# Optimization experiments

Measured on AMD Instinct MI355X. Metric: run time of the kernel, lower is better.

Reference implementation:

```python
import jax, jax.numpy as jnp
import numpy as np

N = 100000      # num_nodes
E = 1600000     # num_edges
F_IN = 128      # node_feature_dim
D_IN = F_IN + 1 # +1 input_cards indicator
H = 128         # hidden dim (both layers)
NUM_CARDS = 110


def _xavier(key, shape):
    fan_out, fan_in = shape
    limit = np.sqrt(6.0 / (fan_in + fan_out))
    return jax.random.uniform(key, shape, jnp.float32, -limit, limit)


def setup_inputs() -> dict:
    key = jax.random.key(0)
    ks = jax.random.split(key, 12)
    x = jax.random.normal(ks[0], (N, F_IN), jnp.float32)
    edge_index = jax.random.randint(ks[1], (2, E), 0, N, jnp.int64)
    input_cards = jax.random.randint(ks[2], (N,), 0, 2, jnp.int32)
    # SAGEConv layer 1: lin_l (neighbors), lin_r (self), each [H, D_IN] + bias
    Wl1 = _xavier(ks[3], (H, D_IN)); bl1 = jnp.zeros((H,), jnp.float32)
    Wr1 = _xavier(ks[4], (H, D_IN)); br1 = jnp.zeros((H,), jnp.float32)
    # SAGEConv layer 2
    Wl2 = _xavier(ks[5], (H, H)); bl2 = jnp.zeros((H,), jnp.float32)
    Wr2 = _xavier(ks[6], (H, H)); br2 = jnp.zeros((H,), jnp.float32)
    # output layer: normal(0, 0.01)
    Wo = 0.01 * jax.random.normal(ks[7], (NUM_CARDS, H), jnp.float32)
    bo = jnp.zeros((NUM_CARDS,), jnp.float32)
    return {"x": x, "Wl1": Wl1, "bl1": bl1, "Wr1": Wr1, "br1": br1,
            "Wl2": Wl2, "bl2": bl2, "Wr2": Wr2, "br2": br2,
            "Wo": Wo, "bo": bo,
            "edge_index": edge_index, "input_cards": input_cards}


def _sage_conv_mean(h, src, dst, deg_inv, Wl, bl, Wr, br):
    # mean-aggregate source-node features at destination nodes
    summed = jax.ops.segment_sum(h[src], dst, num_segments=N)  # [N, d]
    mean = summed * deg_inv[:, None]
    return mean @ Wl.T + bl + h @ Wr.T + br


def reference(x, Wl1, bl1, Wr1, br1, Wl2, bl2, Wr2, br2, Wo, bo,
              edge_index, input_cards):
    src, dst = edge_index[0], edge_index[1]
    deg = jax.ops.segment_sum(jnp.ones((E,), jnp.float32), dst, num_segments=N)
    deg_inv = jnp.where(deg > 0, 1.0 / jnp.maximum(deg, 1.0), 0.0)
    h = jnp.concatenate([x, input_cards.astype(jnp.float32)[:, None]], axis=1)  # [N, D_IN]
    h = jax.nn.relu(_sage_conv_mean(h, src, dst, deg_inv, Wl1, bl1, Wr1, br1))
    h = jax.nn.relu(_sage_conv_mean(h, src, dst, deg_inv, Wl2, bl2, Wr2, br2))
    logits = h @ Wo.T + bo  # [N, NUM_CARDS]
    return logits
```

## Files before the change

### kernel.cpp

```cpp
#include <hip/hip_runtime.h>
#include <hip/hip_bf16.h>

#define N_NODES 100000
#define N_EDGES 1600000
#define HDIM    128
#define KCH     4
#define NUM_CARDS 110
#define NTILES  (N_NODES / 16)
#define GEMM_BLOCKS 1024

#define NB      196
#define MAXB    10240
#define PT      4096
#define PEPT    16

typedef __attribute__((ext_vector_type(8))) short bfrag;
typedef __attribute__((ext_vector_type(4))) float ffrag;
typedef __attribute__((ext_vector_type(2))) float f32x2;

__device__ inline unsigned short f2bf(float f) {
    __hip_bfloat16 h = __float2bfloat16(f);
    unsigned short u; __builtin_memcpy(&u, &h, 2); return u;
}
__device__ inline float bf_lo(unsigned int u) {
    unsigned int v = u << 16; float f; __builtin_memcpy(&f, &v, 4); return f;
}
__device__ inline float bf_hi(unsigned int u) {
    unsigned int v = u & 0xffff0000u; float f; __builtin_memcpy(&f, &v, 4); return f;
}

__device__ inline void gload_lds16(const void* g, void* l) {
    __builtin_amdgcn_global_load_lds(
        (const __attribute__((address_space(1))) unsigned int*)g,
        (__attribute__((address_space(3))) unsigned int*)l, 16, 0, 0);
}


__global__ __launch_bounds__(256) void k_partition(
    const int* __restrict__ src, const int* __restrict__ dst,
    int* __restrict__ bucket_cursor, unsigned int* __restrict__ part) {
    __shared__ int hist[NB];
    __shared__ int hcur[NB];
    const int t = threadIdx.x;
    const int base = blockIdx.x * PT;
    for (int i = t; i < NB; i += 256) hist[i] = 0;
    __syncthreads();
#pragma unroll
    for (int i = 0; i < PEPT; i++) {
        int e = base + i * 256 + t;
        if (e < N_EDGES) atomicAdd(&hist[dst[e] >> 9], 1);
    }
    __syncthreads();
    for (int b = t; b < NB; b += 256) {
        int h = hist[b];
        hcur[b] = h ? atomicAdd(&bucket_cursor[b], h) : 0;
    }
    __syncthreads();
#pragma unroll
    for (int i = 0; i < PEPT; i++) {
        int e = base + i * 256 + t;
        if (e < N_EDGES) {
            int d = dst[e];
            int b = d >> 9;
            int r = atomicAdd(&hcur[b], 1);
            if (r < MAXB)
                part[(size_t)b * MAXB + r] =
                    ((unsigned int)(d & 511) << 17) | (unsigned int)src[e];
        }
    }
}

__global__ __launch_bounds__(256) void k_bucket(
    const unsigned int* __restrict__ part, const int* __restrict__ bucket_cursor,
    int* __restrict__ row_off, int* __restrict__ deg, float* __restrict__ deg_inv,
    int* __restrict__ csr_src) {
    __shared__ int degl[512];
    __shared__ int offl[512];
    __shared__ int curl[512];
    __shared__ int stmp[256];
    const int t = threadIdx.x;
    const int b = blockIdx.x;
    const int n0 = b << 9;
    const int nb = min(512, N_NODES - n0);
    const int cnt = min(bucket_cursor[b], MAXB);
    const int row0 = b * MAXB;
    const unsigned int* pb = &part[(size_t)b * MAXB];

    degl[t] = 0; degl[t + 256] = 0;
    __syncthreads();
    for (int i = t; i < cnt; i += 256)
        atomicAdd(&degl[pb[i] >> 17], 1);
    __syncthreads();
    const int a0 = degl[2 * t], a1 = degl[2 * t + 1];
    stmp[t] = a0 + a1;
    __syncthreads();
    for (int off = 1; off < 256; off <<= 1) {
        int x = (t >= off) ? stmp[t - off] : 0;
        __syncthreads();
        stmp[t] += x;
        __syncthreads();
    }
    const int excl = stmp[t] - (a0 + a1);
    offl[2 * t] = excl;          curl[2 * t] = excl;
    offl[2 * t + 1] = excl + a0; curl[2 * t + 1] = excl + a0;
    __syncthreads();
    for (int i = t; i < nb; i += 256) {
        int n = n0 + i;
        int d = degl[i];
        row_off[n] = row0 + offl[i];
        deg[n] = d;
        deg_inv[n] = (d > 0) ? 1.0f / (float)d : 0.0f;
    }
    for (int i = t; i < cnt; i += 256) {
        unsigned int pk = pb[i];
        int r = atomicAdd(&curl[pk >> 17], 1);
        csr_src[row0 + r] = (int)(pk & 0x1FFFFu);
    }
}


__global__ void k_prep_w(const float* __restrict__ Wl1, const float* __restrict__ Wr1,
                         const float* __restrict__ bl1, const float* __restrict__ br1,
                         const float* __restrict__ Wl2, const float* __restrict__ Wr2,
                         const float* __restrict__ bl2, const float* __restrict__ br2,
                         const float* __restrict__ Wo,  const float* __restrict__ bo,
                         unsigned short* __restrict__ W1, unsigned short* __restrict__ W2,
                         unsigned short* __restrict__ Wob,
                         float* __restrict__ bias1, float* __restrict__ bias2,
                         float* __restrict__ biaso, float* __restrict__ wcard1) {
    const int j = blockIdx.x;
    const int k = threadIdx.x;
    const float* s1 = (j < 128) ? &Wl1[(size_t)j * 129] : &Wr1[(size_t)(j - 128) * 129];
    W1[(size_t)j * HDIM + k] = f2bf(s1[k]);
    const float* s2 = (j < 128) ? &Wl2[(size_t)j * HDIM] : &Wr2[(size_t)(j - 128) * HDIM];
    W2[(size_t)j * HDIM + k] = f2bf(s2[k]);
    if (j < 112)
        Wob[(size_t)j * HDIM + k] = (j < NUM_CARDS) ? f2bf(Wo[(size_t)j * HDIM + k])
                                                    : (unsigned short)0;
    if (k == 0) {
        wcard1[j] = s1[HDIM];
        bias1[j] = (j < 128) ? 0.f : (bl1[j - 128] + br1[j - 128]);
        bias2[j] = (j < 128) ? 0.f : (bl2[j - 128] + br2[j - 128]);
        if (j < 112) biaso[j] = (j < NUM_CARDS) ? bo[j] : 0.f;
    }
}


__global__ __launch_bounds__(256) void k_gemm_dual(
    const unsigned short* __restrict__ Ab, const float* __restrict__ Af,
    const int* __restrict__ cards,
    const unsigned short* __restrict__ W,
    const float* __restrict__ bias, const float* __restrict__ wcard,
    unsigned char* __restrict__ Gq, unsigned short* __restrict__ Rb,
    int layer1) {
    __shared__ __align__(16) unsigned char smem[16384 + 2048];
    float* bias_l = (float*)(smem + 16384);
    float* wc_l   = (float*)(smem + 16384 + 1024);

    const int tix  = threadIdx.x;
    const int wave = tix >> 6;
    const int lane = tix & 63;
    const int m16  = lane & 15;
    const int quad = lane >> 4;
    const int u0   = wave * 4;
    const bool isG = (wave < 2);
    const int xk   = m16 & 7;

    bfrag wf[4][KCH];
#pragma unroll
    for (int u = 0; u < 4; u++) {
        const int j = (u0 + u) * 16 + m16;
#pragma unroll
        for (int c = 0; c < KCH; c++)
            wf[u][c] = *(const bfrag*)&W[(size_t)j * HDIM + c * 32 + quad * 8];
    }

    bias_l[tix] = bias[tix];
    wc_l[tix]   = layer1 ? wcard[tix] : 0.f;

    const int sw1 = (tix ^ ((tix >> 5) & 7)) << 4;
    const int sw2 = (tix ^ ((tix >> 4) & 7)) << 4;
    const int ldsoff = wave << 10;

    int tile = blockIdx.x;
    if (layer1) {
        const unsigned char* g = (const unsigned char*)Af + (size_t)tile * 8192;
        gload_lds16(g + sw1,        smem + ldsoff);
        gload_lds16(g + sw1 + 4096, smem + 4096 + ldsoff);
    } else {
        const unsigned char* g = (const unsigned char*)Ab + (size_t)tile * 4096;
        gload_lds16(g + sw2, smem + ldsoff);
    }
    float cvn = layer1 ? (float)cards[tile * 16 + m16] : 0.f;
    __syncthreads();

    for (int buf = 0; tile < NTILES; tile += GEMM_BLOCKS, buf ^= 1) {
        const int tn = tile + GEMM_BLOCKS;
        const bool more = (tn < NTILES);
        const float cv = cvn;

        if (more) {
            if (layer1) {
                const unsigned char* g = (const unsigned char*)Af + (size_t)tn * 8192;
                unsigned char* d = smem + (buf ^ 1) * 8192 + ldsoff;
                gload_lds16(g + sw1,        d);
                gload_lds16(g + sw1 + 4096, d + 4096);
                cvn = (float)cards[tn * 16 + m16];
            } else {
                const unsigned char* g = (const unsigned char*)Ab + (size_t)tn * 4096;
                gload_lds16(g + sw2, smem + (buf ^ 1) * 4096 + ldsoff);
            }
        }

        const unsigned char* B = smem + buf * (layer1 ? 8192 : 4096);
        bfrag hf[KCH];
        if (layer1) {
#pragma unroll
            for (int c = 0; c < KCH; c++) {
                const int s0 = m16 * 32 + c * 8 + quad * 2;
                const float4 p0 = *(const float4*)(B + (((s0    ) ^ xk) << 4));
                const float4 p1 = *(const float4*)(B + (((s0 + 1) ^ xk) << 4));
                bfrag h;
                h[0] = (short)f2bf(p0.x); h[1] = (short)f2bf(p0.y);
                h[2] = (short)f2bf(p0.z); h[3] = (short)f2bf(p0.w);
                h[4] = (short)f2bf(p1.x); h[5] = (short)f2bf(p1.y);
                h[6] = (short)f2bf(p1.z); h[7] = (short)f2bf(p1.w);
                hf[c] = h;
            }
        } else {
#pragma unroll
            for (int c = 0; c < KCH; c++) {
                const int s = m16 * 16 + c * 4 + quad;
                hf[c] = *(const bfrag*)(B + ((s ^ xk) << 4));
            }
        }

        const int node = tile * 16 + m16;
#pragma unroll
        for (int u = 0; u < 4; u++) {
            ffrag acc = {0.f, 0.f, 0.f, 0.f};
#pragma unroll
            for (int c = 0; c < KCH; c++)
                acc = __builtin_amdgcn_mfma_f32_16x16x32_bf16(wf[u][c], hf[c], acc, 0, 0, 0);
            const int jj0 = (u0 + u) * 16 + quad * 4;
            const float4 b0 = *(const float4*)&bias_l[jj0];
            const float4 w0 = *(const float4*)&wc_l[jj0];
            float v[4];
            v[0] = acc[0] + b0.x + cv * w0.x;
            v[1] = acc[1] + b0.y + cv * w0.y;
            v[2] = acc[2] + b0.z + cv * w0.z;
            v[3] = acc[3] + b0.w + cv * w0.w;
            if (isG) {
                int pk = __builtin_amdgcn_cvt_pk_fp8_f32(v[0], v[1], 0, false);
                pk = __builtin_amdgcn_cvt_pk_fp8_f32(v[2], v[3], pk, true);
                *(unsigned int*)&Gq[(size_t)node * HDIM + (u0 + u) * 16 + quad * 4] =
                    (unsigned int)pk;
            } else {
                unsigned short o[4];
#pragma unroll
                for (int r = 0; r < 4; r++) o[r] = f2bf(v[r]);
                uint2 p = {(unsigned int)o[0] | ((unsigned int)o[1] << 16),
                           (unsigned int)o[2] | ((unsigned int)o[3] << 16)};
                *(uint2*)&Rb[(size_t)node * HDIM + (u0 + u - 8) * 16 + quad * 4] = p;
            }
        }

        if (more) __syncthreads();
    }
}


__global__ __launch_bounds__(256) void k_agg(
    const unsigned char* __restrict__ Gq, const unsigned short* __restrict__ Rb,
    const int* __restrict__ row_off, const int* __restrict__ deg,
    const float* __restrict__ deg_inv, const int* __restrict__ csr_src,
    unsigned short* __restrict__ outH) {
    const int wave = threadIdx.x >> 6;
    const int lane = threadIdx.x & 63;
    const int g = lane >> 3;
    const int l = lane & 7;
    const int n = (blockIdx.x * 4 + wave) * 8 + g;
    const int start = row_off[n];
    const int d = deg[n];
    const float di = deg_inv[n];
    const int fo = l * 16;

    int dmax = d;
    dmax = max(dmax, __shfl_xor(dmax, 8, 64));
    dmax = max(dmax, __shfl_xor(dmax, 16, 64));
    dmax = max(dmax, __shfl_xor(dmax, 32, 64));

    const uint4 rv0 = *(const uint4*)&Rb[(size_t)n * HDIM + fo];
    const uint4 rv1 = *(const uint4*)&Rb[(size_t)n * HDIM + fo + 8];

    f32x2 acc2[8];
#pragma unroll
    for (int i = 0; i < 8; i++) acc2[i] = (f32x2){0.f, 0.f};

    int idxA = (l < d) ? csr_src[start + l] * HDIM : 0;
    int idxB = (8 + l < d) ? csr_src[start + 8 + l] * HDIM : 0;

    uint4 cur = {0u, 0u, 0u, 0u};
    {
        const int off0 = __shfl(idxA, g << 3, 64);
        if (0 < d) cur = *(const uint4*)&Gq[(size_t)(unsigned)off0 + fo];
    }
#define ACC16(Cv)                                                        \
    acc2[0] += __builtin_amdgcn_cvt_pk_f32_fp8((int)(Cv).x, false);      \
    acc2[1] += __builtin_amdgcn_cvt_pk_f32_fp8((int)(Cv).x, true);       \
    acc2[2] += __builtin_amdgcn_cvt_pk_f32_fp8((int)(Cv).y, false);      \
    acc2[3] += __builtin_amdgcn_cvt_pk_f32_fp8((int)(Cv).y, true);       \
    acc2[4] += __builtin_amdgcn_cvt_pk_f32_fp8((int)(Cv).z, false);      \
    acc2[5] += __builtin_amdgcn_cvt_pk_f32_fp8((int)(Cv).z, true);       \
    acc2[6] += __builtin_amdgcn_cvt_pk_f32_fp8((int)(Cv).w, false);      \
    acc2[7] += __builtin_amdgcn_cvt_pk_f32_fp8((int)(Cv).w, true);

    for (int i = 1; i < dmax; i++) {
        const int sl = i & 7;
        if (sl == 0) {
            idxA = idxB;
            const int j = i + 8 + l;
            idxB = (j < d) ? csr_src[start + j] * HDIM : 0;
        }
        const int offn = __shfl(idxA, (g << 3) | sl, 64);
        uint4 nxt = {0u, 0u, 0u, 0u};
        if (i < d) nxt = *(const uint4*)&Gq[(size_t)(unsigned)offn + fo];
        ACC16(cur);
        cur = nxt;
    }
    ACC16(cur);
#undef ACC16

    const float r[16] = {bf_lo(rv0.x), bf_hi(rv0.x), bf_lo(rv0.y), bf_hi(rv0.y),
                         bf_lo(rv0.z), bf_hi(rv0.z), bf_lo(rv0.w), bf_hi(rv0.w),
                         bf_lo(rv1.x), bf_hi(rv1.x), bf_lo(rv1.y), bf_hi(rv1.y),
                         bf_lo(rv1.z), bf_hi(rv1.z), bf_lo(rv1.w), bf_hi(rv1.w)};
    unsigned short o[16];
#pragma unroll
    for (int i = 0; i < 8; i++) {
        o[2 * i]     = f2bf(fmaxf(acc2[i].x * di + r[2 * i], 0.f));
        o[2 * i + 1] = f2bf(fmaxf(acc2[i].y * di + r[2 * i + 1], 0.f));
    }
    uint4 p0, p1;
    p0.x = (unsigned int)o[0] | ((unsigned int)o[1] << 16);
    p0.y = (unsigned int)o[2] | ((unsigned int)o[3] << 16);
    p0.z = (unsigned int)o[4] | ((unsigned int)o[5] << 16);
    p0.w = (unsigned int)o[6] | ((unsigned int)o[7] << 16);
    p1.x = (unsigned int)o[8] | ((unsigned int)o[9] << 16);
    p1.y = (unsigned int)o[10] | ((unsigned int)o[11] << 16);
    p1.z = (unsigned int)o[12] | ((unsigned int)o[13] << 16);
    p1.w = (unsigned int)o[14] | ((unsigned int)o[15] << 16);
    *(uint4*)&outH[(size_t)n * HDIM + fo] = p0;
    *(uint4*)&outH[(size_t)n * HDIM + fo + 8] = p1;
}


__global__ __launch_bounds__(256) void k_gemm_logits(
    const unsigned short* __restrict__ A, const unsigned short* __restrict__ W,
    const float* __restrict__ bias, float* __restrict__ out) {
    __shared__ __align__(16) unsigned char smem[8192];
    const int tix  = threadIdx.x;
    const int wave = tix >> 6;
    const int lane = tix & 63;
    const int m16  = lane & 15;
    const int quad = lane >> 4;
    const int u0   = wave * 2;
    const int xk   = m16 & 7;

    bfrag wf[2][KCH];
    float bsj[2];
#pragma unroll
    for (int u = 0; u < 2; u++) {
        const int unit = u0 + u;
        const int j = (unit < 7 ? unit : 0) * 16 + m16;
#pragma unroll
        for (int c = 0; c < KCH; c++)
            wf[u][c] = *(const bfrag*)&W[(size_t)j * HDIM + c * 32 + quad * 8];
        bsj[u] = bias[j];
    }

    const int sw2 = (tix ^ ((tix >> 4) & 7)) << 4;
    const int ldsoff = wave << 10;

    int tile = blockIdx.x;
    {
        const unsigned char* g = (const unsigned char*)A + (size_t)tile * 4096;
        gload_lds16(g + sw2, smem + ldsoff);
    }
    __syncthreads();

    for (int buf = 0; tile < NTILES; tile += GEMM_BLOCKS, buf ^= 1) {
        const int tn = tile + GEMM_BLOCKS;
        const bool more = (tn < NTILES);
        if (more) {
            const unsigned char* g = (const unsigned char*)A + (size_t)tn * 4096;
            gload_lds16(g + sw2, smem + (buf ^ 1) * 4096 + ldsoff);
        }

        const unsigned char* B = smem + buf * 4096;
        bfrag hf[KCH];
#pragma unroll
        for (int c = 0; c < KCH; c++) {
            const int s = m16 * 16 + c * 4 + quad;
            hf[c] = *(const bfrag*)(B + ((s ^ xk) << 4));
        }

#pragma unroll
        for (int u = 0; u < 2; u++) {
            const int unit = u0 + u;
            if (unit >= 7) break;
            ffrag acc = {0.f, 0.f, 0.f, 0.f};
#pragma unroll
            for (int c = 0; c < KCH; c++)
                acc = __builtin_amdgcn_mfma_f32_16x16x32_bf16(hf[c], wf[u][c], acc, 0, 0, 0);
            const int j = unit * 16 + m16;
            if (j < NUM_CARDS) {
#pragma unroll
                for (int r = 0; r < 4; r++) {
                    const int node = tile * 16 + quad * 4 + r;
                    out[(size_t)node * NUM_CARDS + j] = acc[r] + bsj[u];
                }
            }
        }

        if (more) __syncthreads();
    }
}


static inline size_t align_up(size_t x, size_t a) { return (x + a - 1) & ~(a - 1); }

extern "C" void kernel_launch(void* const* d_in, const int* in_sizes, int n_in,
                              void* d_out, int out_size, void* d_ws, size_t ws_size,
                              hipStream_t stream) {
    const float* x   = (const float*)d_in[0];
    const float* Wl1 = (const float*)d_in[1];
    const float* bl1 = (const float*)d_in[2];
    const float* Wr1 = (const float*)d_in[3];
    const float* br1 = (const float*)d_in[4];
    const float* Wl2 = (const float*)d_in[5];
    const float* bl2 = (const float*)d_in[6];
    const float* Wr2 = (const float*)d_in[7];
    const float* br2 = (const float*)d_in[8];
    const float* Wo  = (const float*)d_in[9];
    const float* bo  = (const float*)d_in[10];
    const int* edge  = (const int*)d_in[11];
    const int* cards = (const int*)d_in[12];
    float* logits = (float*)d_out;

    const int* e_src = edge;
    const int* e_dst = edge + N_EDGES;

    char* w = (char*)d_ws;
    size_t off = 0;
    int* bucket_cursor = (int*)(w + off); off = align_up(off + 256 * 4, 512);
    unsigned int* part = (unsigned int*)(w + off); off = align_up(off + (size_t)NB * MAXB * 4, 512);
    int* row_off = (int*)(w + off); off = align_up(off + N_NODES * 4, 512);
    int* deg_i   = (int*)(w + off); off = align_up(off + N_NODES * 4, 512);
    float* dinv  = (float*)(w + off); off = align_up(off + N_NODES * 4, 512);
    int* csr_src = (int*)(w + off); off = align_up(off + (size_t)NB * MAXB * 4, 512);
    unsigned char*  Gq   = (unsigned char*)(w + off);  off = align_up(off + (size_t)N_NODES * HDIM, 512);
    unsigned short* Rb   = (unsigned short*)(w + off); off = align_up(off + (size_t)N_NODES * HDIM * 2, 512);
    unsigned short* bufH = (unsigned short*)(w + off); off = align_up(off + (size_t)N_NODES * HDIM * 2, 512);
    unsigned short* W1   = (unsigned short*)(w + off); off = align_up(off + 256 * HDIM * 2, 512);
    unsigned short* W2   = (unsigned short*)(w + off); off = align_up(off + 256 * HDIM * 2, 512);
    unsigned short* Wob  = (unsigned short*)(w + off); off = align_up(off + 112 * HDIM * 2, 512);
    float* bias1  = (float*)(w + off); off = align_up(off + 256 * 4, 512);
    float* bias2  = (float*)(w + off); off = align_up(off + 256 * 4, 512);
    float* biaso  = (float*)(w + off); off = align_up(off + 112 * 4, 512);
    float* wcard1 = (float*)(w + off); off = align_up(off + 256 * 4, 512);
    (void)ws_size; (void)n_in; (void)in_sizes; (void)out_size;

    hipMemsetAsync(bucket_cursor, 0, 256 * 4, stream);
    k_prep_w<<<256, 128, 0, stream>>>(Wl1, Wr1, bl1, br1, Wl2, Wr2, bl2, br2, Wo, bo,
                                      W1, W2, Wob, bias1, bias2, biaso, wcard1);

    const int PBLK = (N_EDGES + PT - 1) / PT;
    k_partition<<<PBLK, 256, 0, stream>>>(e_src, e_dst, bucket_cursor, part);
    k_bucket<<<NB, 256, 0, stream>>>(part, bucket_cursor,
                                     row_off, deg_i, dinv, csr_src);

    k_gemm_dual<<<GEMM_BLOCKS, 256, 0, stream>>>(nullptr, x, cards, W1, bias1, wcard1, Gq, Rb, 1);
    k_agg<<<N_NODES / 32, 256, 0, stream>>>(Gq, Rb, row_off, deg_i, dinv, csr_src, bufH);
    k_gemm_dual<<<GEMM_BLOCKS, 256, 0, stream>>>(bufH, nullptr, nullptr, W2, bias2, wcard1, Gq, Rb, 0);
    k_agg<<<N_NODES / 32, 256, 0, stream>>>(Gq, Rb, row_off, deg_i, dinv, csr_src, bufH);
    k_gemm_logits<<<GEMM_BLOCKS, 256, 0, stream>>>(bufH, Wob, biaso, logits);
}
```

Baseline: 317.4 us.

## Co-schedule graph partition/bucketing with layer-1 GEMM and triple-buffer GEMM pipelines

Fuses the edge partition and bucketing kernels with the first-layer GEMM, so each launch runs the graph-preprocessing blocks alongside half of the GEMM tiles and the two kinds of work overlap. The GEMMs switch from double to triple LDS buffering with explicit vmcnt waits and raw barriers, which removes the full syncthreads at the end of each iteration. Layer-2 and logits GEMMs get a dedicated kernel and twice as many blocks. This adds LDS usage and hand-managed waitcnt ordering, and the ordering could be fragile. The partition blocks now also compete for CUs with the GEMM tiles.

New measurement: 311.0 us. 2.0% less time.

```diff
diff --git a/kernel.cpp b/kernel.cpp
--- a/kernel.cpp
+++ b/kernel.cpp
@@ -7,16 +7,21 @@
 #define KCH     4
 #define NUM_CARDS 110
 #define NTILES  (N_NODES / 16)
-#define GEMM_BLOCKS 1024
+#define GB1     1024
+#define HALF1   3125
+#define GB2     2048
 
 #define NB      196
 #define MAXB    10240
 #define PT      4096
 #define PEPT    16
+#define PBLK    ((N_EDGES + PT - 1) / PT)
 
 typedef __attribute__((ext_vector_type(8))) short bfrag;
 typedef __attribute__((ext_vector_type(4))) float ffrag;
 typedef __attribute__((ext_vector_type(2))) float f32x2;
+
+typedef __attribute__((ext_vector_type(2))) unsigned int uint2v;
 
 __device__ inline unsigned short f2bf(float f) {
     __hip_bfloat16 h = __float2bfloat16(f);
@@ -35,14 +40,17 @@
         (__attribute__((address_space(3))) unsigned int*)l, 16, 0, 0);
 }
 
-
-__global__ __launch_bounds__(256) void k_partition(
-    const int* __restrict__ src, const int* __restrict__ dst,
-    int* __restrict__ bucket_cursor, unsigned int* __restrict__ part) {
-    __shared__ int hist[NB];
-    __shared__ int hcur[NB];
+#define SMEM1_SZ (3 * 8192 + 2048 + 256)
+
+
+__device__ void partition_body(
+    int bid, const int* __restrict__ src, const int* __restrict__ dst,
+    int* __restrict__ bucket_cursor, unsigned int* __restrict__ part,
+    unsigned char* smem) {
+    int* hist = (int*)smem;
+    int* hcur = hist + NB;
     const int t = threadIdx.x;
-    const int base = blockIdx.x * PT;
+    const int base = bid * PT;
     for (int i = t; i < NB; i += 256) hist[i] = 0;
     __syncthreads();
 #pragma unroll
@@ -70,16 +78,17 @@
     }
 }
 
-__global__ __launch_bounds__(256) void k_bucket(
-    const unsigned int* __restrict__ part, const int* __restrict__ bucket_cursor,
+__device__ void bucket_body(
+    int bid, const unsigned int* __restrict__ part,
+    const int* __restrict__ bucket_cursor,
     int* __restrict__ row_off, int* __restrict__ deg, float* __restrict__ deg_inv,
-    int* __restrict__ csr_src) {
-    __shared__ int degl[512];
-    __shared__ int offl[512];
-    __shared__ int curl[512];
-    __shared__ int stmp[256];
+    int* __restrict__ csr_src, unsigned char* smem) {
+    int* degl = (int*)smem;
+    int* offl = degl + 512;
+    int* curl = offl + 512;
+    int* stmp = curl + 512;
     const int t = threadIdx.x;
-    const int b = blockIdx.x;
+    const int b = bid;
     const int n0 = b << 9;
     const int nb = min(512, N_NODES - n0);
     const int cnt = min(bucket_cursor[b], MAXB);
@@ -116,6 +125,153 @@
         int r = atomicAdd(&curl[pk >> 17], 1);
         csr_src[row0 + r] = (int)(pk & 0x1FFFFu);
     }
+}
+
+
+__device__ void gemm1_body(
+    int bid, int t0, int tend,
+    const float* __restrict__ Af, const int* __restrict__ cards,
+    const unsigned short* __restrict__ W,
+    const float* __restrict__ bias, const float* __restrict__ wcard,
+    unsigned char* __restrict__ Gq, unsigned short* __restrict__ Rb,
+    unsigned char* smem) {
+    float* bias_l = (float*)(smem + 3 * 8192);
+    float* wc_l   = (float*)(smem + 3 * 8192 + 1024);
+    float* cl     = (float*)(smem + 3 * 8192 + 2048);
+
+    const int tix  = threadIdx.x;
+    const int wave = tix >> 6;
+    const int lane = tix & 63;
+    const int m16  = lane & 15;
+    const int quad = lane >> 4;
+    const int u0   = wave * 4;
+    const bool isG = (wave < 2);
+    const int xk   = m16 & 7;
+
+    bfrag wf[4][KCH];
+#pragma unroll
+    for (int u = 0; u < 4; u++) {
+        const int j = (u0 + u) * 16 + m16;
+#pragma unroll
+        for (int c = 0; c < KCH; c++)
+            wf[u][c] = *(const bfrag*)&W[(size_t)j * HDIM + c * 32 + quad * 8];
+    }
+
+    bias_l[tix] = bias[tix];
+    wc_l[tix]   = wcard[tix];
+    if (tix < 16) {
+#pragma unroll
+        for (int i = 0; i < 4; i++) {
+            const int t = t0 + bid + i * GB1;
+            if (t < tend) cl[i * 16 + tix] = (float)cards[t * 16 + tix];
+        }
+    }
+
+    const int sw = (tix ^ ((tix >> 5) & 7)) << 4;
+    const int ldsoff = wave << 10;
+
+#define STAGE1(T, BI)                                                         \
+    do {                                                                      \
+        const unsigned char* g_ = (const unsigned char*)Af + (size_t)(T) * 8192; \
+        unsigned char* d_ = smem + (BI) * 8192 + ldsoff;                      \
+        gload_lds16(g_ + sw, d_);                                             \
+        gload_lds16(g_ + sw + 4096, d_ + 4096);                               \
+    } while (0)
+
+    int tile = t0 + bid;
+    STAGE1(tile, 0);
+    asm volatile("s_waitcnt lgkmcnt(0)" ::: "memory");
+
+    int b = 0, ic = 0;
+    for (; tile < tend; tile += GB1, ic++) {
+        const int tn = tile + GB1;
+        if (tn < tend) STAGE1(tn, (b == 2 ? 0 : b + 1));
+        asm volatile("s_waitcnt vmcnt(2)" ::: "memory");
+        __builtin_amdgcn_s_barrier();
+        __builtin_amdgcn_sched_barrier(0);
+
+        const float cv = cl[ic * 16 + m16];
+
+        const unsigned char* B = smem + b * 8192;
+        bfrag hf[KCH];
+#pragma unroll
+        for (int c = 0; c < KCH; c++) {
+            const int s0 = m16 * 32 + c * 8 + quad * 2;
+            const float4 p0 = *(const float4*)(B + (((s0    ) ^ xk) << 4));
+            const float4 p1 = *(const float4*)(B + (((s0 + 1) ^ xk) << 4));
+            bfrag h;
+            h[0] = (short)f2bf(p0.x); h[1] = (short)f2bf(p0.y);
+            h[2] = (short)f2bf(p0.z); h[3] = (short)f2bf(p0.w);
+            h[4] = (short)f2bf(p1.x); h[5] = (short)f2bf(p1.y);
+            h[6] = (short)f2bf(p1.z); h[7] = (short)f2bf(p1.w);
+            hf[c] = h;
+        }
+
+        const int node = tile * 16 + m16;
+#pragma unroll
+        for (int u = 0; u < 4; u++) {
+            ffrag acc = {0.f, 0.f, 0.f, 0.f};
+#pragma unroll
+            for (int c = 0; c < KCH; c++)
+                acc = __builtin_amdgcn_mfma_f32_16x16x32_bf16(wf[u][c], hf[c], acc, 0, 0, 0);
+            const int jj0 = (u0 + u) * 16 + quad * 4;
+            const float4 b0 = *(const float4*)&bias_l[jj0];
+            const float4 w0 = *(const float4*)&wc_l[jj0];
+            float v[4];
+            v[0] = acc[0] + b0.x + cv * w0.x;
+            v[1] = acc[1] + b0.y + cv * w0.y;
+            v[2] = acc[2] + b0.z + cv * w0.z;
+            v[3] = acc[3] + b0.w + cv * w0.w;
+            if (isG) {
+                int pk = __builtin_amdgcn_cvt_pk_fp8_f32(v[0], v[1], 0, false);
+                pk = __builtin_amdgcn_cvt_pk_fp8_f32(v[2], v[3], pk, true);
+                *(unsigned int*)&Gq[(size_t)node * HDIM + (u0 + u) * 16 + quad * 4] =
+                    (unsigned int)pk;
+            } else {
+                unsigned short o[4];
+#pragma unroll
+                for (int r = 0; r < 4; r++) o[r] = f2bf(v[r]);
+                uint2 p = {(unsigned int)o[0] | ((unsigned int)o[1] << 16),
+                           (unsigned int)o[2] | ((unsigned int)o[3] << 16)};
+                *(uint2*)&Rb[(size_t)node * HDIM + (u0 + u - 8) * 16 + quad * 4] = p;
+            }
+        }
+        b = (b == 2 ? 0 : b + 1);
+    }
+#undef STAGE1
+}
+
+
+__global__ __launch_bounds__(256) void k_part_gemm1(
+    const int* __restrict__ e_src, const int* __restrict__ e_dst,
+    int* __restrict__ bucket_cursor, unsigned int* __restrict__ part,
+    const float* __restrict__ Af, const int* __restrict__ cards,
+    const unsigned short* __restrict__ W,
+    const float* __restrict__ bias, const float* __restrict__ wcard,
+    unsigned char* __restrict__ Gq, unsigned short* __restrict__ Rb) {
+    __shared__ __align__(16) unsigned char smem[SMEM1_SZ];
+    if (blockIdx.x < PBLK)
+        partition_body(blockIdx.x, e_src, e_dst, bucket_cursor, part, smem);
+    else
+        gemm1_body(blockIdx.x - PBLK, 0, HALF1, Af, cards, W, bias, wcard,
+                   Gq, Rb, smem);
+}
+
+__global__ __launch_bounds__(256) void k_bucket_gemm1(
+    const unsigned int* __restrict__ part, const int* __restrict__ bucket_cursor,
+    int* __restrict__ row_off, int* __restrict__ deg, float* __restrict__ deg_inv,
+    int* __restrict__ csr_src,
+    const float* __restrict__ Af, const int* __restrict__ cards,
+    const unsigned short* __restrict__ W,
+    const float* __restrict__ bias, const float* __restrict__ wcard,
+    unsigned char* __restrict__ Gq, unsigned short* __restrict__ Rb) {
+    __shared__ __align__(16) unsigned char smem[SMEM1_SZ];
+    if (blockIdx.x < NB)
+        bucket_body(blockIdx.x, part, bucket_cursor, row_off, deg, deg_inv,
+                    csr_src, smem);
+    else
+        gemm1_body(blockIdx.x - NB, HALF1, NTILES, Af, cards, W, bias, wcard,
+                   Gq, Rb, smem);
 }
 
 
@@ -146,130 +302,6 @@
 }
 
 
-__global__ __launch_bounds__(256) void k_gemm_dual(
-    const unsigned short* __restrict__ Ab, const float* __restrict__ Af,
-    const int* __restrict__ cards,
-    const unsigned short* __restrict__ W,
-    const float* __restrict__ bias, const float* __restrict__ wcard,
-    unsigned char* __restrict__ Gq, unsigned short* __restrict__ Rb,
-    int layer1) {
-    __shared__ __align__(16) unsigned char smem[16384 + 2048];
-    float* bias_l = (float*)(smem + 16384);
-    float* wc_l   = (float*)(smem + 16384 + 1024);
-
-    const int tix  = threadIdx.x;
-    const int wave = tix >> 6;
-    const int lane = tix & 63;
-    const int m16  = lane & 15;
-    const int quad = lane >> 4;
-    const int u0   = wave * 4;
-    const bool isG = (wave < 2);
-    const int xk   = m16 & 7;
-
-    bfrag wf[4][KCH];
-#pragma unroll
-    for (int u = 0; u < 4; u++) {
-        const int j = (u0 + u) * 16 + m16;
-#pragma unroll
-        for (int c = 0; c < KCH; c++)
-            wf[u][c] = *(const bfrag*)&W[(size_t)j * HDIM + c * 32 + quad * 8];
-    }
-
-    bias_l[tix] = bias[tix];
-    wc_l[tix]   = layer1 ? wcard[tix] : 0.f;
-
-    const int sw1 = (tix ^ ((tix >> 5) & 7)) << 4;
-    const int sw2 = (tix ^ ((tix >> 4) & 7)) << 4;
-    const int ldsoff = wave << 10;
-
-    int tile = blockIdx.x;
-    if (layer1) {
-        const unsigned char* g = (const unsigned char*)Af + (size_t)tile * 8192;
-        gload_lds16(g + sw1,        smem + ldsoff);
-        gload_lds16(g + sw1 + 4096, smem + 4096 + ldsoff);
-    } else {
-        const unsigned char* g = (const unsigned char*)Ab + (size_t)tile * 4096;
-        gload_lds16(g + sw2, smem + ldsoff);
-    }
-    float cvn = layer1 ? (float)cards[tile * 16 + m16] : 0.f;
-    __syncthreads();
-
-    for (int buf = 0; tile < NTILES; tile += GEMM_BLOCKS, buf ^= 1) {
-        const int tn = tile + GEMM_BLOCKS;
-        const bool more = (tn < NTILES);
-        const float cv = cvn;
-
-        if (more) {
-            if (layer1) {
-                const unsigned char* g = (const unsigned char*)Af + (size_t)tn * 8192;
-                unsigned char* d = smem + (buf ^ 1) * 8192 + ldsoff;
-                gload_lds16(g + sw1,        d);
-                gload_lds16(g + sw1 + 4096, d + 4096);
-                cvn = (float)cards[tn * 16 + m16];
-            } else {
-                const unsigned char* g = (const unsigned char*)Ab + (size_t)tn * 4096;
-                gload_lds16(g + sw2, smem + (buf ^ 1) * 4096 + ldsoff);
-            }
-        }
-
-        const unsigned char* B = smem + buf * (layer1 ? 8192 : 4096);
-        bfrag hf[KCH];
-        if (layer1) {
-#pragma unroll
-            for (int c = 0; c < KCH; c++) {
-                const int s0 = m16 * 32 + c * 8 + quad * 2;
-                const float4 p0 = *(const float4*)(B + (((s0    ) ^ xk) << 4));
-                const float4 p1 = *(const float4*)(B + (((s0 + 1) ^ xk) << 4));
-                bfrag h;
-                h[0] = (short)f2bf(p0.x); h[1] = (short)f2bf(p0.y);
-                h[2] = (short)f2bf(p0.z); h[3] = (short)f2bf(p0.w);
-                h[4] = (short)f2bf(p1.x); h[5] = (short)f2bf(p1.y);
-                h[6] = (short)f2bf(p1.z); h[7] = (short)f2bf(p1.w);
-                hf[c] = h;
-            }
-        } else {
-#pragma unroll
-            for (int c = 0; c < KCH; c++) {
-                const int s = m16 * 16 + c * 4 + quad;
-                hf[c] = *(const bfrag*)(B + ((s ^ xk) << 4));
-            }
-        }
-
-        const int node = tile * 16 + m16;
-#pragma unroll
-        for (int u = 0; u < 4; u++) {
-            ffrag acc = {0.f, 0.f, 0.f, 0.f};
-#pragma unroll
-            for (int c = 0; c < KCH; c++)
-                acc = __builtin_amdgcn_mfma_f32_16x16x32_bf16(wf[u][c], hf[c], acc, 0, 0, 0);
-            const int jj0 = (u0 + u) * 16 + quad * 4;
-            const float4 b0 = *(const float4*)&bias_l[jj0];
-            const float4 w0 = *(const float4*)&wc_l[jj0];
-            float v[4];
-            v[0] = acc[0] + b0.x + cv * w0.x;
-            v[1] = acc[1] + b0.y + cv * w0.y;
-            v[2] = acc[2] + b0.z + cv * w0.z;
-            v[3] = acc[3] + b0.w + cv * w0.w;
-            if (isG) {
-                int pk = __builtin_amdgcn_cvt_pk_fp8_f32(v[0], v[1], 0, false);
-                pk = __builtin_amdgcn_cvt_pk_fp8_f32(v[2], v[3], pk, true);
-                *(unsigned int*)&Gq[(size_t)node * HDIM + (u0 + u) * 16 + quad * 4] =
-                    (unsigned int)pk;
-            } else {
-                unsigned short o[4];
-#pragma unroll
-                for (int r = 0; r < 4; r++) o[r] = f2bf(v[r]);
-                uint2 p = {(unsigned int)o[0] | ((unsigned int)o[1] << 16),
-                           (unsigned int)o[2] | ((unsigned int)o[3] << 16)};
-                *(uint2*)&Rb[(size_t)node * HDIM + (u0 + u - 8) * 16 + quad * 4] = p;
-            }
-        }
-
-        if (more) __syncthreads();
-    }
-}
-
-
 __global__ __launch_bounds__(256) void k_agg(
     const unsigned char* __restrict__ Gq, const unsigned short* __restrict__ Rb,
     const int* __restrict__ row_off, const int* __restrict__ deg,
@@ -355,10 +387,94 @@
 }
 
 
+__global__ __launch_bounds__(256) void k_gemm2(
+    const unsigned short* __restrict__ Ab, const unsigned short* __restrict__ W,
+    const float* __restrict__ bias,
+    unsigned char* __restrict__ Gq, unsigned short* __restrict__ Rb) {
+    __shared__ __align__(16) unsigned char smem[3 * 4096 + 1024];
+    float* bias_l = (float*)(smem + 3 * 4096);
+
+    const int tix  = threadIdx.x;
+    const int wave = tix >> 6;
+    const int lane = tix & 63;
+    const int m16  = lane & 15;
+    const int quad = lane >> 4;
+    const int u0   = wave * 4;
+    const bool isG = (wave < 2);
+    const int xk   = m16 & 7;
+
+    bfrag wf[4][KCH];
+#pragma unroll
+    for (int u = 0; u < 4; u++) {
+        const int j = (u0 + u) * 16 + m16;
+#pragma unroll
+        for (int c = 0; c < KCH; c++)
+            wf[u][c] = *(const bfrag*)&W[(size_t)j * HDIM + c * 32 + quad * 8];
+    }
+    bias_l[tix] = bias[tix];
+
+    const int sw = (tix ^ ((tix >> 4) & 7)) << 4;
+    const int ldsoff = wave << 10;
+
+    int tile = blockIdx.x;
+    {
+        const unsigned char* g = (const unsigned char*)Ab + (size_t)tile * 4096;
+        gload_lds16(g + sw, smem + ldsoff);
+    }
+    asm volatile("s_waitcnt lgkmcnt(0)" ::: "memory");
+
+    int b = 0;
+    for (; tile < NTILES; tile += GB2) {
+        const int tn = tile + GB2;
+        if (tn < NTILES) {
+            const unsigned char* g = (const unsigned char*)Ab + (size_t)tn * 4096;
+            gload_lds16(g + sw, smem + (b == 2 ? 0 : b + 1) * 4096 + ldsoff);
+        }
+        asm volatile("s_waitcnt vmcnt(1)" ::: "memory");
+        __builtin_amdgcn_s_barrier();
+        __builtin_amdgcn_sched_barrier(0);
+
+        const unsigned char* B = smem + b * 4096;
+        bfrag hf[KCH];
+#pragma unroll
+        for (int c = 0; c < KCH; c++) {
+            const int s = m16 * 16 + c * 4 + quad;
+            hf[c] = *(const bfrag*)(B + ((s ^ xk) << 4));
+        }
+
+        const int node = tile * 16 + m16;
+#pragma unroll
+        for (int u = 0; u < 4; u++) {
+            ffrag acc = {0.f, 0.f, 0.f, 0.f};
+#pragma unroll
+            for (int c = 0; c < KCH; c++)
+                acc = __builtin_amdgcn_mfma_f32_16x16x32_bf16(wf[u][c], hf[c], acc, 0, 0, 0);
+            const int jj0 = (u0 + u) * 16 + quad * 4;
+            const float4 b0 = *(const float4*)&bias_l[jj0];
+            float v[4] = {acc[0] + b0.x, acc[1] + b0.y, acc[2] + b0.z, acc[3] + b0.w};
+            if (isG) {
+                int pk = __builtin_amdgcn_cvt_pk_fp8_f32(v[0], v[1], 0, false);
+                pk = __builtin_amdgcn_cvt_pk_fp8_f32(v[2], v[3], pk, true);
+                *(unsigned int*)&Gq[(size_t)node * HDIM + (u0 + u) * 16 + quad * 4] =
+                    (unsigned int)pk;
+            } else {
+                unsigned short o[4];
+#pragma unroll
+                for (int r = 0; r < 4; r++) o[r] = f2bf(v[r]);
+                uint2 p = {(unsigned int)o[0] | ((unsigned int)o[1] << 16),
+                           (unsigned int)o[2] | ((unsigned int)o[3] << 16)};
+                *(uint2*)&Rb[(size_t)node * HDIM + (u0 + u - 8) * 16 + quad * 4] = p;
+            }
+        }
+        b = (b == 2 ? 0 : b + 1);
+    }
+}
+
+
 __global__ __launch_bounds__(256) void k_gemm_logits(
     const unsigned short* __restrict__ A, const unsigned short* __restrict__ W,
     const float* __restrict__ bias, float* __restrict__ out) {
-    __shared__ __align__(16) unsigned char smem[8192];
+    __shared__ __align__(16) unsigned char smem[3 * 4096];
     const int tix  = threadIdx.x;
     const int wave = tix >> 6;
     const int lane = tix & 63;
@@ -387,17 +503,19 @@
         const unsigned char* g = (const unsigned char*)A + (size_t)tile * 4096;
         gload_lds16(g + sw2, smem + ldsoff);
     }
-    __syncthreads();
-
-    for (int buf = 0; tile < NTILES; tile += GEMM_BLOCKS, buf ^= 1) {
-        const int tn = tile + GEMM_BLOCKS;
-        const bool more = (tn < NTILES);
-        if (more) {
+
+    int b = 0;
+    for (; tile < NTILES; tile += GB2) {
+        const int tn = tile + GB2;
+        if (tn < NTILES) {
             const unsigned char* g = (const unsigned char*)A + (size_t)tn * 4096;
-            gload_lds16(g + sw2, smem + (buf ^ 1) * 4096 + ldsoff);
-        }
-
-        const unsigned char* B = smem + buf * 4096;
+            gload_lds16(g + sw2, smem + (b == 2 ? 0 : b + 1) * 4096 + ldsoff);
+        }
+        asm volatile("s_waitcnt vmcnt(1)" ::: "memory");
+        __builtin_amdgcn_s_barrier();
+        __builtin_amdgcn_sched_barrier(0);
+
+        const unsigned char* B = smem + b * 4096;
         bfrag hf[KCH];
 #pragma unroll
         for (int c = 0; c < KCH; c++) {
@@ -422,8 +540,7 @@
                 }
             }
         }
-
-        if (more) __syncthreads();
+        b = (b == 2 ? 0 : b + 1);
     }
 }
 
@@ -475,14 +592,15 @@
     k_prep_w<<<256, 128, 0, stream>>>(Wl1, Wr1, bl1, br1, Wl2, Wr2, bl2, br2, Wo, bo,
                                       W1, W2, Wob, bias1, bias2, biaso, wcard1);
 
-    const int PBLK = (N_EDGES + PT - 1) / PT;
-    k_partition<<<PBLK, 256, 0, stream>>>(e_src, e_dst, bucket_cursor, part);
-    k_bucket<<<NB, 256, 0, stream>>>(part, bucket_cursor,
-                                     row_off, deg_i, dinv, csr_src);
-
-    k_gemm_dual<<<GEMM_BLOCKS, 256, 0, stream>>>(nullptr, x, cards, W1, bias1, wcard1, Gq, Rb, 1);
+    k_part_gemm1<<<PBLK + GB1, 256, 0, stream>>>(
+        e_src, e_dst, bucket_cursor, part,
+        x, cards, W1, bias1, wcard1, Gq, Rb);
+    k_bucket_gemm1<<<NB + GB1, 256, 0, stream>>>(
+        part, bucket_cursor, row_off, deg_i, dinv, csr_src,
+        x, cards, W1, bias1, wcard1, Gq, Rb);
+
     k_agg<<<N_NODES / 32, 256, 0, stream>>>(Gq, Rb, row_off, deg_i, dinv, csr_src, bufH);
-    k_gemm_dual<<<GEMM_BLOCKS, 256, 0, stream>>>(bufH, nullptr, nullptr, W2, bias2, wcard1, Gq, Rb, 0);
+    k_gemm2<<<GB2, 256, 0, stream>>>(bufH, W2, bias2, Gq, Rb);
     k_agg<<<N_NODES / 32, 256, 0, stream>>>(Gq, Rb, row_off, deg_i, dinv, csr_src, bufH);
-    k_gemm_logits<<<GEMM_BLOCKS, 256, 0, stream>>>(bufH, Wob, biaso, logits);
-}
+    k_gemm_logits<<<GB2, 256, 0, stream>>>(bufH, Wob, biaso, logits);
+}
```
